# Kernel tuning notes

Measured on AMD Instinct MI355X. Metric: run time of the kernel, lower is better.

Reference implementation:

```python
import jax, jax.numpy as jnp
import numpy as np


def _conv(x, w):
    # NCHW 'same' conv, stride 1 (kernel 7 -> pad 3 each side)
    return jax.lax.conv_general_dilated(
        x, w, window_strides=(1, 1), padding='SAME',
        dimension_numbers=('NCHW', 'OIHW', 'NCHW'))


def _run_dir(x, w_ih, w_hh, b, reverse):
    # x: (B, T, C, H, W); returns (B, T, hid, H, W)
    B, T, C, H, W = x.shape
    hid = w_hh.shape[1]
    # Precompute input-to-gate convs for all timesteps at once (fold T into batch)
    xg = _conv(x.reshape(B * T, C, H, W), w_ih) + b[None, :, None, None]
    xg = xg.reshape(B, T, 4 * hid, H, W).transpose(1, 0, 2, 3, 4)  # (T,B,4hid,H,W)
    h0 = jnp.zeros((B, hid, H, W), x.dtype)
    c0 = jnp.zeros_like(h0)

    def step(carry, g_x):
        h, c = carry
        g = g_x + _conv(h, w_hh)
        i, f, gg, o = jnp.split(g, 4, axis=1)  # PyTorch LSTM gate order
        c = jax.nn.sigmoid(f) * c + jax.nn.sigmoid(i) * jnp.tanh(gg)
        h = jax.nn.sigmoid(o) * jnp.tanh(c)
        return (h, c), h

    _, hs = jax.lax.scan(step, (h0, c0), xg, reverse=reverse)
    return hs.transpose(1, 0, 2, 3, 4)  # (B,T,hid,H,W)


def setup_inputs() -> dict:
    key = jax.random.key(0)
    ks = jax.random.split(key, 6)
    B, T, C, H, W = 8, 16, 3, 32, 32
    hid, K = 64, 7
    s_ih = 1.0 / np.sqrt(C * K * K)
    s_hh = 1.0 / np.sqrt(hid * K * K)
    return {
        'x': jax.random.normal(ks[0], (B, T, C, H, W), jnp.float32),
        'w_ih_f': jax.random.normal(ks[1], (4 * hid, C, K, K), jnp.float32) * s_ih,
        'w_hh_f': jax.random.normal(ks[2], (4 * hid, hid, K, K), jnp.float32) * s_hh,
        'b_f': jnp.zeros((4 * hid,), jnp.float32),
        'w_ih_b': jax.random.normal(ks[3], (4 * hid, C, K, K), jnp.float32) * s_ih,
        'w_hh_b': jax.random.normal(ks[4], (4 * hid, hid, K, K), jnp.float32) * s_hh,
        'b_b': jnp.zeros((4 * hid,), jnp.float32),
    }


def reference(x, w_ih_f, w_hh_f, b_f, w_ih_b, w_hh_b, b_b):
    out_f = _run_dir(x, w_ih_f, w_hh_f, b_f, reverse=False)
    out_b = _run_dir(x, w_ih_b, w_hh_b, b_b, reverse=True)
    # bidirectional concat along channel dim -> (B, T, 2*hid, H, W)
    return jnp.concatenate([out_f, out_b], axis=2)
```

## Files before the change

### kernel.cpp

```cpp
#include <hip/hip_runtime.h>
#include <hip/hip_bf16.h>


#define HP0_B  0
#define HP1_B  3112960
#define C_B    6225920
#define WALL_B 10420224
#define BIAS_B 13860864
#define FLAG_B 13862912

using short8 = __attribute__((ext_vector_type(8))) short;
using f32x4  = __attribute__((ext_vector_type(4))) float;

__device__ __forceinline__ float sigm(float x) { return 1.0f / (1.0f + __expf(-x)); }
__device__ __forceinline__ float tanh_f(float x) {
    x = fminf(fmaxf(x, -30.0f), 30.0f);
    float e = __expf(2.0f * x);
    return (e - 1.0f) / (e + 1.0f);
}

__global__ void detect_dtype(const unsigned int* __restrict__ xw, int* __restrict__ flag) {
    int lane = threadIdx.x;
    int cnt = 0;
    for (int i = 0; i < 4; ++i) {
        unsigned int w = xw[lane * 4 + i];
        unsigned int e = (w >> 7) & 0xFFu;
        cnt += (e >= 0xC0u) ? 1 : 0;
    }
#pragma unroll
    for (int off = 32; off > 0; off >>= 1) cnt += __shfl_down(cnt, off, 64);
    if (lane == 0) *flag = (cnt > 16) ? 1 : 0;
}

__global__ void prep_weights(const void* __restrict__ whhf, const void* __restrict__ whhb,
                             const void* __restrict__ wihf, const void* __restrict__ wihb,
                             const void* __restrict__ bf, const void* __restrict__ bb,
                             short* __restrict__ wall, float* __restrict__ bias_r,
                             const int* __restrict__ flag) {
    int n = blockIdx.x * blockDim.x + threadIdx.x;
    const int fp32 = *flag;
    if (n < 1720320) {
        int icl = n & 31;
        int oc = (n >> 5) & 255;
        int ks = (n >> 13) % 105;
        int d = n / 860160;
        const void* hh = d ? whhb : whhf;
        const void* ih = d ? wihb : wihf;
        float v = 0.0f;
        if (ks < 98) {
            int ky = ks / 14, rr = ks % 14, kc = rr / 7, kx = rr % 7;
            int si = ((oc * 64 + kc * 32 + icl) * 7 + ky) * 7 + kx;
            v = fp32 ? ((const float*)hh)[si] : __bfloat162float(((const __hip_bfloat16*)hh)[si]);
        } else {
            int kx = ks - 98, ky = icl >> 2, ic = icl & 3;
            if (ic < 3 && ky < 7) {
                int si = ((oc * 3 + ic) * 7 + ky) * 7 + kx;
                v = fp32 ? ((const float*)ih)[si] : __bfloat162float(((const __hip_bfloat16*)ih)[si]);
            }
        }
        __hip_bfloat16 hv = __float2bfloat16(v);
        wall[n] = *(short*)&hv;
        return;
    }
    n -= 1720320;
    if (n < 512) {
        const void* src = (n >= 256) ? bb : bf;
        int j = n & 255;
        bias_r[n] = fp32 ? ((const float*)src)[j] : __bfloat162float(((const __hip_bfloat16*)src)[j]);
    }
}

__global__ void zero_state(float* __restrict__ ws_f) {
    int n = blockIdx.x * blockDim.x + threadIdx.x;
    if (n < 2605056) ws_f[n] = 0.0f;
}

__global__ __launch_bounds__(256, 1)
void lstm_step(const void* __restrict__ xin,
               const short* __restrict__ wall,
               const float* __restrict__ bias_r,
               const unsigned short* __restrict__ hp_r,
               unsigned short* __restrict__ hp_w,
               float* __restrict__ c,
               void* __restrict__ out,
               const int* __restrict__ flag, int s) {
    const int ygrp = blockIdx.x;
    const int b = blockIdx.y;
    const int dir = blockIdx.z;
    const int t = dir ? (15 - s) : s;
    const int y0 = ygrp * 2;
    const int tid = threadIdx.x;
    const int w = tid >> 6;
    const int l = tid & 63;
    const int q = l >> 4;
    const int li = l & 15;
    const int fp32 = *flag;
    const int db = dir * 8 + b;

    __shared__ short lds[23040 + 3200];

    {
        const uint4* src = (const uint4*)(hp_r + (size_t)(db * 38 + y0) * 40 * 64);
        for (int i = tid; i < 2560; i += 256) {
            int ic8 = i & 7, col = (i >> 3) % 40, row = i / 320;
            uint4 v = src[i];
            *(uint4*)&lds[(row * 40 + col) * 72 + ic8 * 8] = v;
        }
    }
    for (int i = tid; i < 3200; i += 256) {
        int k = i % 40, cc = (i / 40) % 40, r = i / 1600;
        float v = 0.0f;
        if (k < 28) {
            int ky = k >> 2, ic = k & 3;
            int yin = y0 + r + ky - 3, cin = cc - 3;
            if (ic < 3 && yin >= 0 && yin < 32 && cin >= 0 && cin < 32) {
                size_t gi = (size_t)((b * 16 + t) * 3 + ic) * 1024 + yin * 32 + cin;
                v = fp32 ? ((const float*)xin)[gi]
                         : __bfloat162float(((const __hip_bfloat16*)xin)[gi]);
            }
        }
        __hip_bfloat16 hb = __float2bfloat16(v);
        lds[23040 + i] = *(short*)&hb;
    }
    __syncthreads();

    f32x4 acc[4][4];
    {
        const float* bp = bias_r + dir * 256 + w * 16 + q * 4;
#pragma unroll
        for (int g = 0; g < 4; ++g) {
            f32x4 bv = *(const f32x4*)(bp + g * 64);
#pragma unroll
            for (int nt = 0; nt < 4; ++nt) acc[g][nt] = bv;
        }
    }

    const short* wbase = wall + (size_t)dir * 860160 + ((w * 16 + li) * 32 + q * 8);
    int bh[4], bx[4];
#pragma unroll
    for (int nt = 0; nt < 4; ++nt) {
        int rt = nt >> 1, ct = nt & 1;
        bh[nt] = (rt * 40 + ct * 16 + li) * 72 + q * 8;
        bx[nt] = 23040 + (rt * 40 + ct * 16 + li) * 40 + q * 8;
    }

    auto loadA = [&](short8* A, int ks) {
        const short* p = wbase + (size_t)ks * 8192;
#pragma unroll
        for (int g = 0; g < 4; ++g) A[g] = *(const short8*)(p + g * 2048);
    };
    auto loadB = [&](short8* B, int ks) {
        if (ks < 98) {
            int ky = ks / 14, rr = ks % 14;
            int uoff = ky * 2880 + (rr % 7) * 72 + (rr / 7) * 32;
#pragma unroll
            for (int nt = 0; nt < 4; ++nt) B[nt] = *(const short8*)&lds[bh[nt] + uoff];
        } else {
            int uoff = (ks - 98) * 40;
#pragma unroll
            for (int nt = 0; nt < 4; ++nt) B[nt] = *(const short8*)&lds[bx[nt] + uoff];
        }
    };
    auto mfma16 = [&](short8* A, short8* B) {
#pragma unroll
        for (int g = 0; g < 4; ++g)
#pragma unroll
            for (int nt = 0; nt < 4; ++nt)
                acc[g][nt] = __builtin_amdgcn_mfma_f32_16x16x32_bf16(A[g], B[nt], acc[g][nt], 0, 0, 0);
    };

    short8 A0[4], A1[4], B0[4], B1[4];
    loadA(A0, 0); loadB(B0, 0);
#pragma unroll 1
    for (int ks = 0; ks < 104; ks += 2) {
        loadA(A1, ks + 1); loadB(B1, ks + 1);
        mfma16(A0, B0);
        loadA(A0, ks + 2); loadB(B0, ks + 2);
        mfma16(A1, B1);
    }
    mfma16(A0, B0);

    const int hid0 = w * 16 + q * 4;
#pragma unroll
    for (int nt = 0; nt < 4; ++nt) {
        int y = y0 + (nt >> 1);
        int px = (nt & 1) * 16 + li;
        float* cp = c + (size_t)(db * 1024 + y * 32 + px) * 64 + hid0;
        f32x4 cold = *(const f32x4*)cp;
        f32x4 hv;
#pragma unroll
        for (int r = 0; r < 4; ++r) {
            float iv = sigm(acc[0][nt][r]);
            float fv = sigm(acc[1][nt][r]);
            float gv = tanh_f(acc[2][nt][r]);
            float ov = sigm(acc[3][nt][r]);
            float cn = fv * cold[r] + iv * gv;
            cold[r] = cn;
            hv[r] = ov * tanh_f(cn);
        }
        *(f32x4*)cp = cold;

        ushort4 hu;
        {
            __hip_bfloat16 t0 = __float2bfloat16(hv[0]); hu.x = *(unsigned short*)&t0;
            __hip_bfloat16 t1 = __float2bfloat16(hv[1]); hu.y = *(unsigned short*)&t1;
            __hip_bfloat16 t2 = __float2bfloat16(hv[2]); hu.z = *(unsigned short*)&t2;
            __hip_bfloat16 t3 = __float2bfloat16(hv[3]); hu.w = *(unsigned short*)&t3;
        }
        *(ushort4*)(hp_w + (size_t)((db * 38 + y + 3) * 40 + px + 3) * 64 + hid0) = hu;

        size_t ob = (size_t)((b * 16 + t) * 128 + dir * 64 + hid0) * 1024 + y * 32 + px;
        if (fp32) {
            float* op = (float*)out;
#pragma unroll
            for (int r = 0; r < 4; ++r) op[ob + (size_t)r * 1024] = hv[r];
        } else {
            __hip_bfloat16* op = (__hip_bfloat16*)out;
#pragma unroll
            for (int r = 0; r < 4; ++r) op[ob + (size_t)r * 1024] = __float2bfloat16(hv[r]);
        }
    }
}

extern "C" void kernel_launch(void* const* d_in, const int* in_sizes, int n_in,
                              void* d_out, int out_size, void* d_ws, size_t ws_size,
                              hipStream_t stream) {
    char* wsb = (char*)d_ws;
    unsigned short* hp0 = (unsigned short*)(wsb + HP0_B);
    unsigned short* hp1 = (unsigned short*)(wsb + HP1_B);
    float* c = (float*)(wsb + C_B);
    short* wall = (short*)(wsb + WALL_B);
    float* bias_r = (float*)(wsb + BIAS_B);
    int* flag = (int*)(wsb + FLAG_B);

    detect_dtype<<<1, 64, 0, stream>>>((const unsigned int*)d_in[0], flag);
    prep_weights<<<6722, 256, 0, stream>>>(d_in[2], d_in[5], d_in[1], d_in[4],
                                           d_in[3], d_in[6], wall, bias_r, flag);
    zero_state<<<10176, 256, 0, stream>>>((float*)d_ws);

    for (int s = 0; s < 16; ++s) {
        unsigned short* hr = (s & 1) ? hp1 : hp0;
        unsigned short* hw = (s & 1) ? hp0 : hp1;
        lstm_step<<<dim3(16, 8, 2), 256, 0, stream>>>(d_in[0], wall, bias_r,
                                                      hr, hw, c, d_out, flag, s);
    }
}
```

Before: 661.8 us.

## Split the K reduction across two wave groups with an LDS partial-sum exchange

```diff
diff --git a/kernel.cpp b/kernel.cpp
--- a/kernel.cpp
+++ b/kernel.cpp
@@ -75,7 +75,7 @@
     if (n < 2605056) ws_f[n] = 0.0f;
 }
 
-__global__ __launch_bounds__(256, 1)
+__global__ __launch_bounds__(512, 2)
 void lstm_step(const void* __restrict__ xin,
                const short* __restrict__ wall,
                const float* __restrict__ bias_r,
@@ -90,24 +90,26 @@
     const int t = dir ? (15 - s) : s;
     const int y0 = ygrp * 2;
     const int tid = threadIdx.x;
-    const int w = tid >> 6;
+    const int wv = tid >> 6;
+    const int kg = wv >> 2;
+    const int wm = wv & 3;
     const int l = tid & 63;
     const int q = l >> 4;
     const int li = l & 15;
     const int fp32 = *flag;
     const int db = dir * 8 + b;
 
-    __shared__ short lds[23040 + 3200];
+    __shared__ __align__(16) short lds[26240];
 
     {
         const uint4* src = (const uint4*)(hp_r + (size_t)(db * 38 + y0) * 40 * 64);
-        for (int i = tid; i < 2560; i += 256) {
+        for (int i = tid; i < 2560; i += 512) {
             int ic8 = i & 7, col = (i >> 3) % 40, row = i / 320;
             uint4 v = src[i];
             *(uint4*)&lds[(row * 40 + col) * 72 + ic8 * 8] = v;
         }
     }
-    for (int i = tid; i < 3200; i += 256) {
+    for (int i = tid; i < 3200; i += 512) {
         int k = i % 40, cc = (i / 40) % 40, r = i / 1600;
         float v = 0.0f;
         if (k < 28) {
@@ -125,17 +127,23 @@
     __syncthreads();
 
     f32x4 acc[4][4];
-    {
-        const float* bp = bias_r + dir * 256 + w * 16 + q * 4;
+    if (kg == 0) {
+        const float* bp = bias_r + dir * 256 + wm * 16 + q * 4;
 #pragma unroll
         for (int g = 0; g < 4; ++g) {
             f32x4 bv = *(const f32x4*)(bp + g * 64);
 #pragma unroll
             for (int nt = 0; nt < 4; ++nt) acc[g][nt] = bv;
         }
-    }
-
-    const short* wbase = wall + (size_t)dir * 860160 + ((w * 16 + li) * 32 + q * 8);
+    } else {
+        f32x4 z = {0.0f, 0.0f, 0.0f, 0.0f};
+#pragma unroll
+        for (int g = 0; g < 4; ++g)
+#pragma unroll
+            for (int nt = 0; nt < 4; ++nt) acc[g][nt] = z;
+    }
+
+    const short* wbase = wall + (size_t)dir * 860160 + ((wm * 16 + li) * 32 + q * 8);
     int bh[4], bx[4];
 #pragma unroll
     for (int nt = 0; nt < 4; ++nt) {
@@ -169,18 +177,49 @@
                 acc[g][nt] = __builtin_amdgcn_mfma_f32_16x16x32_bf16(A[g], B[nt], acc[g][nt], 0, 0, 0);
     };
 
+    const int ks_begin = kg ? 52 : 0;
+    const int ks_end   = kg ? 105 : 52;
     short8 A0[4], A1[4], B0[4], B1[4];
-    loadA(A0, 0); loadB(B0, 0);
+    loadA(A0, ks_begin); loadB(B0, ks_begin);
+    int ks = ks_begin;
 #pragma unroll 1
-    for (int ks = 0; ks < 104; ks += 2) {
+    for (; ks + 1 < ks_end; ks += 2) {
         loadA(A1, ks + 1); loadB(B1, ks + 1);
         mfma16(A0, B0);
-        loadA(A0, ks + 2); loadB(B0, ks + 2);
+        int kn = (ks + 2 < ks_end) ? ks + 2 : ks;
+        loadA(A0, kn); loadB(B0, kn);
         mfma16(A1, B1);
     }
-    mfma16(A0, B0);
-
-    const int hid0 = w * 16 + q * 4;
+    if (ks < ks_end) mfma16(A0, B0);
+
+    __syncthreads();
+    {
+        float* exch = (float*)lds;
+#pragma unroll 1
+        for (int half = 0; half < 2; ++half) {
+            if (kg == 1) {
+                float* xp = exch + wm * 2048 + q * 64 + li * 4;
+#pragma unroll
+                for (int g = 0; g < 2; ++g)
+#pragma unroll
+                    for (int nt = 0; nt < 4; ++nt)
+                        *(f32x4*)(xp + (g * 4 + nt) * 256) = acc[2 * half + g][nt];
+            }
+            __syncthreads();
+            if (kg == 0) {
+                const float* xp = exch + wm * 2048 + q * 64 + li * 4;
+#pragma unroll
+                for (int g = 0; g < 2; ++g)
+#pragma unroll
+                    for (int nt = 0; nt < 4; ++nt)
+                        acc[2 * half + g][nt] += *(const f32x4*)(xp + (g * 4 + nt) * 256);
+            }
+            __syncthreads();
+        }
+    }
+    if (kg == 1) return;
+
+    const int hid0 = wm * 16 + q * 4;
 #pragma unroll
     for (int nt = 0; nt < 4; ++nt) {
         int y = y0 + (nt >> 1);
@@ -241,7 +280,7 @@
     for (int s = 0; s < 16; ++s) {
         unsigned short* hr = (s & 1) ? hp1 : hp0;
         unsigned short* hw = (s & 1) ? hp0 : hp1;
-        lstm_step<<<dim3(16, 8, 2), 256, 0, stream>>>(d_in[0], wall, bias_r,
+        lstm_step<<<dim3(16, 8, 2), 512, 0, stream>>>(d_in[0], wall, bias_r,
                                                       hr, hw, c, d_out, flag, s);
     }
 }
```

Result: slower. 927.3 us (+40.1%).
